# Kernel tuning notes

Measured on AMD Instinct MI355X. Metric: run time of the kernel, lower is better.

## Reference

```python
import jax, jax.numpy as jnp
import numpy as np

B, S, D = 2, 2048, 1024
H = 16
HD = D // H  # 64
SCALE = HD ** -0.5


def setup_inputs() -> dict:
    key = jax.random.key(0)
    ks = jax.random.split(key, 9)
    init = lambda k, shape: jax.random.normal(k, shape, dtype=jnp.float32) * (1.0 / np.sqrt(shape[-1]))
    return {
        "x": jax.random.normal(ks[0], (B, S, D), dtype=jnp.float32),
        "wq": init(ks[1], (D, D)), "bq": jnp.zeros((D,), jnp.float32),
        "wk": init(ks[2], (D, D)), "bk": jnp.zeros((D,), jnp.float32),
        "wv": init(ks[3], (D, D)), "bv": jnp.zeros((D,), jnp.float32),
        "wo": init(ks[4], (D, D)), "bo": jnp.zeros((D,), jnp.float32),
    }


def reference(x, wq, bq, wk, bk, wv, bv, wo, bo):
    b, s, d = x.shape
    # projections -> [b, h, s, hd]
    q = (x @ wq + bq).reshape(b, s, H, HD).transpose(0, 2, 1, 3)
    k = (x @ wk + bk).reshape(b, s, H, HD).transpose(0, 2, 1, 3)
    v = (x @ wv + bv).reshape(b, s, H, HD).transpose(0, 2, 1, 3)
    # full causal attention (chunked loop in original computes exactly this)
    scores = jnp.einsum("bhqd,bhkd->bhqk", q, k) * SCALE
    causal = jnp.tril(jnp.ones((s, s), dtype=bool))
    scores = jnp.where(causal, scores, -jnp.inf)
    weights = jax.nn.softmax(scores, axis=-1)
    out = jnp.einsum("bhqk,bhkd->bhqd", weights, v)
    out = out.transpose(0, 2, 1, 3).reshape(b, s, d)
    return out @ wo + bo
```

## Files before the change

### kernel.cpp

```cpp
#include <hip/hip_runtime.h>
#include <hip/hip_bf16.h>
#include <cstdint>

#define B_  2
#define S_  2048
#define D_  1024
#define H_  16
#define HD_ 64
#define M_  (B_ * S_)
static constexpr float SC_LOG2E = 0.125f * 1.44269504088896f;

typedef __bf16 bf16x8 __attribute__((ext_vector_type(8)));
typedef __bf16 bf16x4 __attribute__((ext_vector_type(4)));
typedef float  f32x4  __attribute__((ext_vector_type(4)));

__device__ __forceinline__ unsigned short f2b(float f) {
  union { float f; unsigned u; } x; x.f = f;
  unsigned r = x.u + 0x7FFF + ((x.u >> 16) & 1);
  return (unsigned short)(r >> 16);
}

__device__ __forceinline__ void gl_lds16(const unsigned short* g, unsigned short* l) {
  __builtin_amdgcn_global_load_lds((const __attribute__((address_space(1))) void*)g,
                                   (__attribute__((address_space(3))) void*)l, 16, 0, 0);
}

__device__ __forceinline__ void bar_lgkm() {
  asm volatile("s_waitcnt lgkmcnt(0)\n\ts_barrier" ::: "memory");
}
__device__ __forceinline__ void bar_vm2() {
  asm volatile("s_waitcnt vmcnt(2) lgkmcnt(0)\n\ts_barrier" ::: "memory");
}
__device__ __forceinline__ void bar_vm0() {
  asm volatile("s_waitcnt vmcnt(0) lgkmcnt(0)\n\ts_barrier" ::: "memory");
}

__global__ void cvt_all_kernel(const float* __restrict__ x,
                               const float* __restrict__ w0, const float* __restrict__ w1,
                               const float* __restrict__ w2, const float* __restrict__ w3,
                               unsigned short* __restrict__ xb,
                               unsigned short* __restrict__ o0, unsigned short* __restrict__ o1,
                               unsigned short* __restrict__ o2, unsigned short* __restrict__ o3) {
  int tx = threadIdx.x, ty = threadIdx.y;
  if (blockIdx.z == 4) {
    int tid = ty * 32 + tx;
    int base = ((int)blockIdx.y * 32 + (int)blockIdx.x) * 1024 + tid;
    const float4* xf = (const float4*)x;
    ushort4* ob = (ushort4*)xb;
#pragma unroll
    for (int j = 0; j < 4; j++) {
      float4 v = xf[base + j * 256];
      ushort4 r;
      r.x = f2b(v.x); r.y = f2b(v.y); r.z = f2b(v.z); r.w = f2b(v.w);
      ob[base + j * 256] = r;
    }
    return;
  }
  const float* w = blockIdx.z == 0 ? w0 : blockIdx.z == 1 ? w1 : blockIdx.z == 2 ? w2 : w3;
  unsigned short* o = blockIdx.z == 0 ? o0 : blockIdx.z == 1 ? o1 : blockIdx.z == 2 ? o2 : o3;
  __shared__ float t[32][33];
  int x0 = blockIdx.x * 32, y0 = blockIdx.y * 32;
#pragma unroll
  for (int j = 0; j < 4; j++)
    t[ty + j * 8][tx] = w[(size_t)(y0 + ty + j * 8) * D_ + x0 + tx];
  __syncthreads();
#pragma unroll
  for (int j = 0; j < 4; j++)
    o[(size_t)(x0 + ty + j * 8) * D_ + y0 + tx] = f2b(t[tx][ty + j * 8]);
}

__global__ __launch_bounds__(512) void qkv_gemm_kernel(
    const unsigned short* __restrict__ xb,
    const unsigned short* __restrict__ wqt, const unsigned short* __restrict__ wkt,
    const unsigned short* __restrict__ wvt,
    const float* __restrict__ bq, const float* __restrict__ bk, const float* __restrict__ bv,
    unsigned short* __restrict__ qo, unsigned short* __restrict__ ko, unsigned short* __restrict__ vo) {
  const unsigned short* wt = blockIdx.z == 0 ? wqt : blockIdx.z == 1 ? wkt : wvt;
  const float* bias        = blockIdx.z == 0 ? bq  : blockIdx.z == 1 ? bk  : bv;
  unsigned short* out      = blockIdx.z == 0 ? qo  : blockIdx.z == 1 ? ko  : vo;
  const float scl = blockIdx.z == 0 ? SC_LOG2E : 1.0f;

  __shared__ __align__(16) unsigned short smem[6 * 4096];
  const int tid = threadIdx.x;
  const int lane = tid & 63, wid = tid >> 6;
  const int wm = wid & 1, wn = wid >> 1;
  const int m0 = blockIdx.x * 128, n0 = blockIdx.y * 128;
  const int l15 = lane & 15, q4 = lane >> 4;
  const int srow = tid >> 2, skc = (tid & 3) * 8;

  f32x4 zero = {0.f, 0.f, 0.f, 0.f};
  f32x4 acc[4][2];
#pragma unroll
  for (int mt = 0; mt < 4; mt++)
#pragma unroll
    for (int nt = 0; nt < 2; nt++) acc[mt][nt] = zero;

  const unsigned short* ap = xb + (size_t)(m0 + srow) * D_ + skc;
  const unsigned short* bp = wt + (size_t)(n0 + srow) * D_ + skc;
  gl_lds16(ap,      smem + tid * 8);
  gl_lds16(bp,      smem + 12288 + tid * 8);
  gl_lds16(ap + 32, smem + 4096 + tid * 8);
  gl_lds16(bp + 32, smem + 12288 + 4096 + tid * 8);

  int bc = 0;
  for (int it = 0; it < 32; it++) {
    if (it < 31) bar_vm2(); else bar_vm0();
    if (it + 2 < 32) {
      int bn_ = bc < 1 ? bc + 2 : bc - 1;
      gl_lds16(ap + (it + 2) * 32, smem + bn_ * 4096 + tid * 8);
      gl_lds16(bp + (it + 2) * 32, smem + 12288 + bn_ * 4096 + tid * 8);
    }
    const unsigned short* Ab = smem + bc * 4096;
    const unsigned short* Bb = smem + 12288 + bc * 4096;
    bf16x8 af[4], bfv[2];
#pragma unroll
    for (int mt = 0; mt < 4; mt++) af[mt]  = *(const bf16x8*)(Ab + (wm * 64 + mt * 16 + l15) * 32 + q4 * 8);
#pragma unroll
    for (int nt = 0; nt < 2; nt++) bfv[nt] = *(const bf16x8*)(Bb + (wn * 32 + nt * 16 + l15) * 32 + q4 * 8);
#pragma unroll
    for (int mt = 0; mt < 4; mt++)
#pragma unroll
      for (int nt = 0; nt < 2; nt++)
        acc[mt][nt] = __builtin_amdgcn_mfma_f32_16x16x32_bf16(af[mt], bfv[nt], acc[mt][nt], 0, 0, 0);
    bc = bc == 2 ? 0 : bc + 1;
  }

  if (blockIdx.z < 2) {
#pragma unroll
    for (int nt = 0; nt < 2; nt++) {
      int n = n0 + wn * 32 + nt * 16 + l15;
      float bn = bias[n];
      int h = n >> 6, hd = n & 63;
#pragma unroll
      for (int mt = 0; mt < 4; mt++) {
#pragma unroll
        for (int r = 0; r < 4; r++) {
          int m = m0 + wm * 64 + mt * 16 + q4 * 4 + r;
          int b = m >> 11, s = m & (S_ - 1);
          out[(((size_t)(b * H_ + h)) * S_ + s) * HD_ + hd] = f2b((acc[mt][nt][r] + bn) * scl);
        }
      }
    }
  } else {
    unsigned short* buf = smem;
#pragma unroll
    for (int p = 0; p < 2; p++) {
      __syncthreads();
      if ((wn >> 1) == p) {
#pragma unroll
        for (int nt = 0; nt < 2; nt++) {
          int np = (wn & 1) * 32 + nt * 16 + l15;
          float bn = bias[n0 + p * 64 + np];
#pragma unroll
          for (int mt = 0; mt < 4; mt++) {
            f32x4 vb = acc[mt][nt];
            vb[0] += bn; vb[1] += bn; vb[2] += bn; vb[3] += bn;
            bf16x4 pk = __builtin_convertvector(vb, bf16x4);
            *(bf16x4*)(&buf[np * 136 + wm * 64 + mt * 16 + q4 * 4]) = pk;
          }
        }
      }
      __syncthreads();
#pragma unroll
      for (int i = 0; i < 2; i++) {
        int ci = tid + i * 512;
        int np = ci >> 4, c = ci & 15;
        int n = n0 + p * 64 + np;
        int h = n >> 6, hd = n & 63;
        int m = m0 + c * 8;
        int b = m >> 11, s = m & (S_ - 1);
        *(uint4*)(out + (((size_t)(b * H_ + h)) * HD_ + hd) * S_ + s) = *(const uint4*)(buf + np * 136 + c * 8);
      }
    }
  }
}

__global__ __launch_bounds__(512) void attn_kernel(
    const unsigned short* __restrict__ Q, const unsigned short* __restrict__ K,
    const unsigned short* __restrict__ Vt_g, unsigned short* __restrict__ O) {
  const int bh = blockIdx.y, b = bh >> 4, h = bh & 15;
  const unsigned short* Qh = Q    + (size_t)bh * S_ * HD_;
  const unsigned short* Kh = K    + (size_t)bh * S_ * HD_;
  const unsigned short* Vh = Vt_g + (size_t)bh * HD_ * S_;

  __shared__ __align__(16) unsigned short Ks[2][128 * 72];
  __shared__ __align__(16) unsigned short Vt[2][64 * 136];
  __shared__ __align__(16) unsigned short Ps[8][16 * 136];

  const int tid = threadIdx.x, lane = tid & 63, w = tid >> 6;
  const int l15 = lane & 15, q4 = lane >> 4;
  f32x4 zero = {0.f, 0.f, 0.f, 0.f};

  const int krow0 = tid >> 3, kcol0 = (tid & 7) * 8;
  const int vrow0 = tid >> 4, vcol0 = (tid & 15) * 8;

  int tc = 0;
  for (int half = 0; half < 2; half++) {
    const int qi = half ? (15 - (int)blockIdx.x) : (int)blockIdx.x;
    const int q0 = qi * 128;

    const unsigned short* qp = Qh + (size_t)(q0 + w * 16 + l15) * HD_ + q4 * 8;
    bf16x8 bq0 = *(const bf16x8*)(qp);
    bf16x8 bq1 = *(const bf16x8*)(qp + 32);

    float m_i = -1e30f, l_i = 0.f;
    f32x4 o_acc[4];
#pragma unroll
    for (int t = 0; t < 4; t++) o_acc[t] = zero;
    const int qrow = q0 + w * 16 + l15;
    const int nkt = qi + 1;

    uint4 kp0 = *(const uint4*)(Kh + (size_t)krow0 * HD_ + kcol0);
    uint4 kp1 = *(const uint4*)(Kh + (size_t)(krow0 + 64) * HD_ + kcol0);
    uint4 vp0 = *(const uint4*)(Vh + (size_t)vrow0 * S_ + vcol0);
    uint4 vp1 = *(const uint4*)(Vh + (size_t)(vrow0 + 32) * S_ + vcol0);

    for (int kt = 0; kt < nkt; kt++, tc++) {
      const int k0 = kt * 128;
      const int bi = tc & 1;
      unsigned short* Kb = Ks[bi];
      unsigned short* Vb = Vt[bi];
      *(uint4*)(Kb + krow0 * 72 + kcol0) = kp0;
      *(uint4*)(Kb + (krow0 + 64) * 72 + kcol0) = kp1;
      *(uint4*)(Vb + vrow0 * 136 + vcol0) = vp0;
      *(uint4*)(Vb + (vrow0 + 32) * 136 + vcol0) = vp1;
      bar_lgkm();
      if (kt + 1 < nkt) {
        int kn = k0 + 128;
        kp0 = *(const uint4*)(Kh + (size_t)(kn + krow0) * HD_ + kcol0);
        kp1 = *(const uint4*)(Kh + (size_t)(kn + krow0 + 64) * HD_ + kcol0);
        vp0 = *(const uint4*)(Vh + (size_t)vrow0 * S_ + kn + vcol0);
        vp1 = *(const uint4*)(Vh + (size_t)(vrow0 + 32) * S_ + kn + vcol0);
      }

      f32x4 sc[8];
#pragma unroll
      for (int nt = 0; nt < 8; nt++) sc[nt] = zero;
#pragma unroll
      for (int nt = 0; nt < 8; nt++) {
        bf16x8 ak0 = *(const bf16x8*)(Kb + (nt * 16 + l15) * 72 + q4 * 8);
        bf16x8 ak1 = *(const bf16x8*)(Kb + (nt * 16 + l15) * 72 + 32 + q4 * 8);
        sc[nt] = __builtin_amdgcn_mfma_f32_16x16x32_bf16(ak0, bq0, sc[nt], 0, 0, 0);
        sc[nt] = __builtin_amdgcn_mfma_f32_16x16x32_bf16(ak1, bq1, sc[nt], 0, 0, 0);
      }

      const bool needMask = (k0 + 127) > (q0 + w * 16);
      float mx = m_i;
      if (needMask) {
#pragma unroll
        for (int nt = 0; nt < 8; nt++)
#pragma unroll
          for (int r = 0; r < 4; r++) {
            int key = k0 + nt * 16 + q4 * 4 + r;
            float v = (key > qrow) ? -1e30f : sc[nt][r];
            sc[nt][r] = v;
            mx = fmaxf(mx, v);
          }
      } else {
#pragma unroll
        for (int nt = 0; nt < 8; nt++)
#pragma unroll
          for (int r = 0; r < 4; r++) mx = fmaxf(mx, sc[nt][r]);
      }
      mx = fmaxf(mx, __shfl_xor(mx, 16));
      mx = fmaxf(mx, __shfl_xor(mx, 32));
      float alpha = __builtin_amdgcn_exp2f(m_i - mx);
      m_i = mx;
      float rs = 0.f;
#pragma unroll
      for (int nt = 0; nt < 8; nt++)
#pragma unroll
        for (int r = 0; r < 4; r++) {
          float p = __builtin_amdgcn_exp2f(sc[nt][r] - mx);
          sc[nt][r] = p;
          rs += p;
        }
      rs += __shfl_xor(rs, 16);
      rs += __shfl_xor(rs, 32);
      l_i = l_i * alpha + rs;

#pragma unroll
      for (int r = 0; r < 4; r++) {
        float ar = __shfl(alpha, q4 * 4 + r);
        o_acc[0][r] *= ar; o_acc[1][r] *= ar; o_acc[2][r] *= ar; o_acc[3][r] *= ar;
      }

#pragma unroll
      for (int nt = 0; nt < 8; nt++) {
        bf16x4 pk = __builtin_convertvector(sc[nt], bf16x4);
        *(bf16x4*)(&Ps[w][l15 * 136 + nt * 16 + q4 * 4]) = pk;
      }
      __threadfence_block();

#pragma unroll
      for (int ks = 0; ks < 4; ks++) {
        bf16x8 ap = *(const bf16x8*)(&Ps[w][l15 * 136 + ks * 32 + q4 * 8]);
#pragma unroll
        for (int nt2 = 0; nt2 < 4; nt2++) {
          bf16x8 bv = *(const bf16x8*)(Vb + (nt2 * 16 + l15) * 136 + ks * 32 + q4 * 8);
          o_acc[nt2] = __builtin_amdgcn_mfma_f32_16x16x32_bf16(ap, bv, o_acc[nt2], 0, 0, 0);
        }
      }
    }

#pragma unroll
    for (int r = 0; r < 4; r++) {
      float lr = __shfl(l_i, q4 * 4 + r);
      float inv = 1.0f / lr;
      int s = q0 + w * 16 + q4 * 4 + r;
#pragma unroll
      for (int nt2 = 0; nt2 < 4; nt2++)
        O[((size_t)(b * S_ + s)) * D_ + h * HD_ + nt2 * 16 + l15] = f2b(o_acc[nt2][r] * inv);
    }
  }
}

__global__ __launch_bounds__(512) void out_gemm_kernel(
    const unsigned short* __restrict__ ab, const unsigned short* __restrict__ wot,
    const float* __restrict__ bo, float* __restrict__ out) {
  __shared__ __align__(16) unsigned short smem[6 * 4096];
  const int tid = threadIdx.x;
  const int lane = tid & 63, wid = tid >> 6;
  const int wm = wid & 1, wn = wid >> 1;
  const int m0 = blockIdx.x * 128, n0 = blockIdx.y * 128;
  const int l15 = lane & 15, q4 = lane >> 4;
  const int srow = tid >> 2, skc = (tid & 3) * 8;

  f32x4 zero = {0.f, 0.f, 0.f, 0.f};
  f32x4 acc[4][2];
#pragma unroll
  for (int mt = 0; mt < 4; mt++)
#pragma unroll
    for (int nt = 0; nt < 2; nt++) acc[mt][nt] = zero;

  const unsigned short* ap = ab  + (size_t)(m0 + srow) * D_ + skc;
  const unsigned short* bp = wot + (size_t)(n0 + srow) * D_ + skc;
  gl_lds16(ap,      smem + tid * 8);
  gl_lds16(bp,      smem + 12288 + tid * 8);
  gl_lds16(ap + 32, smem + 4096 + tid * 8);
  gl_lds16(bp + 32, smem + 12288 + 4096 + tid * 8);

  int bc = 0;
  for (int it = 0; it < 32; it++) {
    if (it < 31) bar_vm2(); else bar_vm0();
    if (it + 2 < 32) {
      int bn_ = bc < 1 ? bc + 2 : bc - 1;
      gl_lds16(ap + (it + 2) * 32, smem + bn_ * 4096 + tid * 8);
      gl_lds16(bp + (it + 2) * 32, smem + 12288 + bn_ * 4096 + tid * 8);
    }
    const unsigned short* Ab = smem + bc * 4096;
    const unsigned short* Bb = smem + 12288 + bc * 4096;
    bf16x8 af[4], bfv[2];
#pragma unroll
    for (int mt = 0; mt < 4; mt++) af[mt]  = *(const bf16x8*)(Ab + (wm * 64 + mt * 16 + l15) * 32 + q4 * 8);
#pragma unroll
    for (int nt = 0; nt < 2; nt++) bfv[nt] = *(const bf16x8*)(Bb + (wn * 32 + nt * 16 + l15) * 32 + q4 * 8);
#pragma unroll
    for (int mt = 0; mt < 4; mt++)
#pragma unroll
      for (int nt = 0; nt < 2; nt++)
        acc[mt][nt] = __builtin_amdgcn_mfma_f32_16x16x32_bf16(af[mt], bfv[nt], acc[mt][nt], 0, 0, 0);
    bc = bc == 2 ? 0 : bc + 1;
  }

#pragma unroll
  for (int nt = 0; nt < 2; nt++) {
    int n = n0 + wn * 32 + nt * 16 + l15;
    float bn = bo[n];
#pragma unroll
    for (int mt = 0; mt < 4; mt++) {
#pragma unroll
      for (int r = 0; r < 4; r++) {
        int m = m0 + wm * 64 + mt * 16 + q4 * 4 + r;
        out[(size_t)m * D_ + n] = acc[mt][nt][r] + bn;
      }
    }
  }
}

extern "C" void kernel_launch(void* const* d_in, const int* in_sizes, int n_in,
                              void* d_out, int out_size, void* d_ws, size_t ws_size,
                              hipStream_t stream) {
  const float* x  = (const float*)d_in[0];
  const float* wq = (const float*)d_in[1];
  const float* bq = (const float*)d_in[2];
  const float* wk = (const float*)d_in[3];
  const float* bk = (const float*)d_in[4];
  const float* wv = (const float*)d_in[5];
  const float* bv = (const float*)d_in[6];
  const float* wo = (const float*)d_in[7];
  const float* bo = (const float*)d_in[8];
  float* out = (float*)d_out;

  char* ws = (char*)d_ws;
  unsigned short* xb  = (unsigned short*)(ws);
  unsigned short* wqt = (unsigned short*)(ws + (8u  << 20));
  unsigned short* wkt = (unsigned short*)(ws + (10u << 20));
  unsigned short* wvt = (unsigned short*)(ws + (12u << 20));
  unsigned short* wot = (unsigned short*)(ws + (14u << 20));
  unsigned short* qb  = (unsigned short*)(ws + (16u << 20));
  unsigned short* kb  = (unsigned short*)(ws + (24u << 20));
  unsigned short* vtg = (unsigned short*)(ws + (32u << 20));
  unsigned short* ab  = xb;

  cvt_all_kernel<<<dim3(32, 32, 5), dim3(32, 8), 0, stream>>>(x, wq, wk, wv, wo, xb, wqt, wkt, wvt, wot);
  qkv_gemm_kernel<<<dim3(32, 8, 3), dim3(512), 0, stream>>>(xb, wqt, wkt, wvt, bq, bk, bv, qb, kb, vtg);
  attn_kernel<<<dim3(8, B_ * H_), dim3(512), 0, stream>>>(qb, kb, vtg, ab);
  out_gemm_kernel<<<dim3(32, 8), dim3(512), 0, stream>>>(ab, wot, bo, out);
}
```

Baseline: 180.3 us.

## Split attention KV tiles across two wave groups with merge, swizzled LDS

The attention kernel now launches 1024-thread blocks in which two groups of eight waves each process alternating 128-key tiles for the same query rows. Each group keeps its own online-softmax state, and the two states are merged through LDS scratch at the end. The change also XOR-swizzles the K/V LDS layout in place of padding, and skips the output rescale when the running max grows by less than a threshold. It interleaves the P stores with the PV MFMAs, adds s_setprio around MFMA blocks, and flattens the grid with head-major block ordering. The aim is to double key-dimension parallelism and cut LDS bank conflicts, at the cost of extra barriers, a merge step, and higher register and LDS pressure.

```diff
diff --git a/kernel.cpp b/kernel.cpp
--- a/kernel.cpp
+++ b/kernel.cpp
@@ -175,143 +175,206 @@
   }
 }
 
-__global__ __launch_bounds__(512) void attn_kernel(
+__global__ __launch_bounds__(1024, 4) void attn_kernel(
     const unsigned short* __restrict__ Q, const unsigned short* __restrict__ K,
     const unsigned short* __restrict__ Vt_g, unsigned short* __restrict__ O) {
-  const int bh = blockIdx.y, b = bh >> 4, h = bh & 15;
+  const int id = blockIdx.x;
+  const int bh = id & 31, x = id >> 5;
+  const int b = bh >> 4, h = bh & 15;
   const unsigned short* Qh = Q    + (size_t)bh * S_ * HD_;
   const unsigned short* Kh = K    + (size_t)bh * S_ * HD_;
   const unsigned short* Vh = Vt_g + (size_t)bh * HD_ * S_;
 
-  __shared__ __align__(16) unsigned short Ks[2][128 * 72];
-  __shared__ __align__(16) unsigned short Vt[2][64 * 136];
-  __shared__ __align__(16) unsigned short Ps[8][16 * 136];
+  __shared__ __align__(16) unsigned short Ks[2][2][128 * 64];
+  __shared__ __align__(16) unsigned short Vt[2][2][64 * 128];
+  __shared__ __align__(16) unsigned short Ps[16][640];
 
   const int tid = threadIdx.x, lane = tid & 63, w = tid >> 6;
+  const int hi = w >> 3, qw = w & 7;
   const int l15 = lane & 15, q4 = lane >> 4;
+  const int st = tid >> 9, sid = tid & 511;
+  const int krow0 = sid >> 3, kcol0 = (sid & 7) * 8;
+  const int vrow0 = sid >> 4, vcol0 = (sid & 15) * 8;
+  const int kc0s = kcol0 ^ ((krow0 & 7) << 3);
+  const int vc0s = vcol0 ^ ((vrow0 & 7) << 3);
+  const int kx = (l15 & 7) << 3;
+  const int kcA = (q4 * 8) ^ kx, kcB = (q4 * 8 + 32) ^ kx;
+  unsigned short* Pw = &Ps[w][0];
+  const int pw0 = l15 * 40 + q4 * 4;
+  const int pr0 = l15 * 40 + q4 * 8;
+  float* scr = (float*)&Ks[0][0][0];
+  float* sp = scr + (size_t)(qw * 64 + lane) * 20;
+
   f32x4 zero = {0.f, 0.f, 0.f, 0.f};
-
-  const int krow0 = tid >> 3, kcol0 = (tid & 7) * 8;
-  const int vrow0 = tid >> 4, vcol0 = (tid & 15) * 8;
-
-  int tc = 0;
-  for (int half = 0; half < 2; half++) {
-    const int qi = half ? (15 - (int)blockIdx.x) : (int)blockIdx.x;
+  int stc = 0;
+
+  for (int hf = 0; hf < 2; hf++) {
+    const int qi = hf ? 15 - x : x;
     const int q0 = qi * 128;
-
-    const unsigned short* qp = Qh + (size_t)(q0 + w * 16 + l15) * HD_ + q4 * 8;
+    const int nkt = qi + 1, nst = (nkt + 1) >> 1;
+
+    const unsigned short* qp = Qh + (size_t)(q0 + qw * 16 + l15) * HD_ + q4 * 8;
     bf16x8 bq0 = *(const bf16x8*)(qp);
     bf16x8 bq1 = *(const bf16x8*)(qp + 32);
+    const int qrow = q0 + qw * 16 + l15;
 
     float m_i = -1e30f, l_i = 0.f;
     f32x4 o_acc[4];
 #pragma unroll
-    for (int t = 0; t < 4; t++) o_acc[t] = zero;
-    const int qrow = q0 + w * 16 + l15;
-    const int nkt = qi + 1;
-
-    uint4 kp0 = *(const uint4*)(Kh + (size_t)krow0 * HD_ + kcol0);
-    uint4 kp1 = *(const uint4*)(Kh + (size_t)(krow0 + 64) * HD_ + kcol0);
-    uint4 vp0 = *(const uint4*)(Vh + (size_t)vrow0 * S_ + vcol0);
-    uint4 vp1 = *(const uint4*)(Vh + (size_t)(vrow0 + 32) * S_ + vcol0);
-
-    for (int kt = 0; kt < nkt; kt++, tc++) {
-      const int k0 = kt * 128;
-      const int bi = tc & 1;
-      unsigned short* Kb = Ks[bi];
-      unsigned short* Vb = Vt[bi];
-      *(uint4*)(Kb + krow0 * 72 + kcol0) = kp0;
-      *(uint4*)(Kb + (krow0 + 64) * 72 + kcol0) = kp1;
-      *(uint4*)(Vb + vrow0 * 136 + vcol0) = vp0;
-      *(uint4*)(Vb + (vrow0 + 32) * 136 + vcol0) = vp1;
+    for (int t4 = 0; t4 < 4; t4++) o_acc[t4] = zero;
+
+    uint4 kp0 = {0,0,0,0}, kp1 = {0,0,0,0}, vp0 = {0,0,0,0}, vp1 = {0,0,0,0};
+    if (st < nkt) {
+      const int k0p = st * 128;
+      kp0 = *(const uint4*)(Kh + (size_t)(k0p + krow0) * HD_ + kcol0);
+      kp1 = *(const uint4*)(Kh + (size_t)(k0p + krow0 + 64) * HD_ + kcol0);
+      vp0 = *(const uint4*)(Vh + (size_t)vrow0 * S_ + k0p + vcol0);
+      vp1 = *(const uint4*)(Vh + (size_t)(vrow0 + 32) * S_ + k0p + vcol0);
+    }
+
+    for (int s = 0; s < nst; s++, stc++) {
+      const int buf = stc & 1;
+      {
+        unsigned short* Kb = &Ks[buf][st][0];
+        unsigned short* Vb = &Vt[buf][st][0];
+        *(uint4*)(Kb + krow0 * 64 + kc0s) = kp0;
+        *(uint4*)(Kb + (krow0 + 64) * 64 + kc0s) = kp1;
+        *(uint4*)(Vb + vrow0 * 128 + vc0s) = vp0;
+        *(uint4*)(Vb + (vrow0 + 32) * 128 + vc0s) = vp1;
+      }
       bar_lgkm();
-      if (kt + 1 < nkt) {
-        int kn = k0 + 128;
-        kp0 = *(const uint4*)(Kh + (size_t)(kn + krow0) * HD_ + kcol0);
-        kp1 = *(const uint4*)(Kh + (size_t)(kn + krow0 + 64) * HD_ + kcol0);
-        vp0 = *(const uint4*)(Vh + (size_t)vrow0 * S_ + kn + vcol0);
-        vp1 = *(const uint4*)(Vh + (size_t)(vrow0 + 32) * S_ + kn + vcol0);
-      }
-
-      f32x4 sc[8];
-#pragma unroll
-      for (int nt = 0; nt < 8; nt++) sc[nt] = zero;
-#pragma unroll
-      for (int nt = 0; nt < 8; nt++) {
-        bf16x8 ak0 = *(const bf16x8*)(Kb + (nt * 16 + l15) * 72 + q4 * 8);
-        bf16x8 ak1 = *(const bf16x8*)(Kb + (nt * 16 + l15) * 72 + 32 + q4 * 8);
-        sc[nt] = __builtin_amdgcn_mfma_f32_16x16x32_bf16(ak0, bq0, sc[nt], 0, 0, 0);
-        sc[nt] = __builtin_amdgcn_mfma_f32_16x16x32_bf16(ak1, bq1, sc[nt], 0, 0, 0);
-      }
-
-      const bool needMask = (k0 + 127) > (q0 + w * 16);
-      float mx = m_i;
-      if (needMask) {
+      const int ktn = 2 * (s + 1) + st;
+      if (ktn < nkt) {
+        const int k0n = ktn * 128;
+        kp0 = *(const uint4*)(Kh + (size_t)(k0n + krow0) * HD_ + kcol0);
+        kp1 = *(const uint4*)(Kh + (size_t)(k0n + krow0 + 64) * HD_ + kcol0);
+        vp0 = *(const uint4*)(Vh + (size_t)vrow0 * S_ + k0n + vcol0);
+        vp1 = *(const uint4*)(Vh + (size_t)(vrow0 + 32) * S_ + k0n + vcol0);
+      }
+
+      const int kt = 2 * s + hi;
+      if (kt < nkt) {
+        const int k0 = kt * 128;
+        const unsigned short* Kb = &Ks[buf][hi][0];
+        const unsigned short* Vb = &Vt[buf][hi][0];
+
+        f32x4 sc[8];
+#pragma unroll
+        for (int nt = 0; nt < 8; nt++) sc[nt] = zero;
+        __builtin_amdgcn_s_setprio(1);
+#pragma unroll
+        for (int nt = 0; nt < 8; nt++) {
+          bf16x8 ak0 = *(const bf16x8*)(Kb + (nt * 16 + l15) * 64 + kcA);
+          bf16x8 ak1 = *(const bf16x8*)(Kb + (nt * 16 + l15) * 64 + kcB);
+          sc[nt] = __builtin_amdgcn_mfma_f32_16x16x32_bf16(ak0, bq0, sc[nt], 0, 0, 0);
+          sc[nt] = __builtin_amdgcn_mfma_f32_16x16x32_bf16(ak1, bq1, sc[nt], 0, 0, 0);
+        }
+        __builtin_amdgcn_s_setprio(0);
+
+        if ((k0 + 127) > (q0 + qw * 16)) {
+#pragma unroll
+          for (int nt = 0; nt < 8; nt++)
+#pragma unroll
+            for (int r = 0; r < 4; r++) {
+              int key = k0 + nt * 16 + q4 * 4 + r;
+              if (key > qrow) sc[nt][r] = -1e30f;
+            }
+        }
+
+        float am[8];
 #pragma unroll
         for (int nt = 0; nt < 8; nt++)
+          am[nt] = fmaxf(fmaxf(sc[nt][0], sc[nt][1]), fmaxf(sc[nt][2], sc[nt][3]));
+#pragma unroll
+        for (int sr = 4; sr > 0; sr >>= 1)
+#pragma unroll
+          for (int i2 = 0; i2 < sr; i2++) am[i2] = fmaxf(am[i2], am[i2 + sr]);
+        float mx = am[0];
+        mx = fmaxf(mx, __shfl_xor(mx, 16));
+        mx = fmaxf(mx, __shfl_xor(mx, 32));
+        mx = fmaxf(mx, m_i);
+
+        if (!__all(mx - m_i <= 10.0f)) {
+          float alpha = __builtin_amdgcn_exp2f(m_i - mx);
+          m_i = mx;
+          l_i *= alpha;
 #pragma unroll
           for (int r = 0; r < 4; r++) {
-            int key = k0 + nt * 16 + q4 * 4 + r;
-            float v = (key > qrow) ? -1e30f : sc[nt][r];
-            sc[nt][r] = v;
-            mx = fmaxf(mx, v);
+            float ar = __shfl(alpha, q4 * 4 + r);
+            o_acc[0][r] *= ar; o_acc[1][r] *= ar; o_acc[2][r] *= ar; o_acc[3][r] *= ar;
           }
-      } else {
-#pragma unroll
-        for (int nt = 0; nt < 8; nt++)
-#pragma unroll
-          for (int r = 0; r < 4; r++) mx = fmaxf(mx, sc[nt][r]);
-      }
-      mx = fmaxf(mx, __shfl_xor(mx, 16));
-      mx = fmaxf(mx, __shfl_xor(mx, 32));
-      float alpha = __builtin_amdgcn_exp2f(m_i - mx);
-      m_i = mx;
-      float rs = 0.f;
-#pragma unroll
-      for (int nt = 0; nt < 8; nt++)
-#pragma unroll
-        for (int r = 0; r < 4; r++) {
-          float p = __builtin_amdgcn_exp2f(sc[nt][r] - mx);
-          sc[nt][r] = p;
-          rs += p;
-        }
-      rs += __shfl_xor(rs, 16);
-      rs += __shfl_xor(rs, 32);
-      l_i = l_i * alpha + rs;
-
+        }
+
+        float sm[8];
+#pragma unroll
+        for (int nt = 0; nt < 8; nt++) {
+          f32x4 pv;
+#pragma unroll
+          for (int r = 0; r < 4; r++) pv[r] = __builtin_amdgcn_exp2f(sc[nt][r] - m_i);
+          sc[nt] = pv;
+          sm[nt] = (pv[0] + pv[1]) + (pv[2] + pv[3]);
+        }
+#pragma unroll
+        for (int sr = 4; sr > 0; sr >>= 1)
+#pragma unroll
+          for (int i2 = 0; i2 < sr; i2++) sm[i2] += sm[i2 + sr];
+        float rs = sm[0];
+        rs += __shfl_xor(rs, 16);
+        rs += __shfl_xor(rs, 32);
+        l_i += rs;
+
+#pragma unroll
+        for (int ks = 0; ks < 4; ks++) {
+          bf16x4 pk0 = __builtin_convertvector(sc[2 * ks],     bf16x4);
+          bf16x4 pk1 = __builtin_convertvector(sc[2 * ks + 1], bf16x4);
+          *(bf16x4*)(Pw + pw0)      = pk0;
+          *(bf16x4*)(Pw + pw0 + 16) = pk1;
+          __threadfence_block();
+          bf16x8 ap2 = *(const bf16x8*)(Pw + pr0);
+          __builtin_amdgcn_s_setprio(1);
+#pragma unroll
+          for (int nt2 = 0; nt2 < 4; nt2++) {
+            bf16x8 bv = *(const bf16x8*)(Vb + (nt2 * 16 + l15) * 128 + ((ks * 32 + q4 * 8) ^ kx));
+            o_acc[nt2] = __builtin_amdgcn_mfma_f32_16x16x32_bf16(ap2, bv, o_acc[nt2], 0, 0, 0);
+          }
+          __builtin_amdgcn_s_setprio(0);
+        }
+      }
+    }
+
+    bar_lgkm();
+    if (hi) {
+      *(f32x4*)(sp + 0)  = o_acc[0];
+      *(f32x4*)(sp + 4)  = o_acc[1];
+      *(f32x4*)(sp + 8)  = o_acc[2];
+      *(f32x4*)(sp + 12) = o_acc[3];
+      sp[16] = m_i; sp[17] = l_i;
+    }
+    bar_lgkm();
+    if (!hi) {
+      f32x4 oh[4];
+      oh[0] = *(const f32x4*)(sp + 0);
+      oh[1] = *(const f32x4*)(sp + 4);
+      oh[2] = *(const f32x4*)(sp + 8);
+      oh[3] = *(const f32x4*)(sp + 12);
+      float m_h = sp[16], l_h = sp[17];
+      float M   = fmaxf(m_i, m_h);
+      float a_l = __builtin_amdgcn_exp2f(m_i - M);
+      float a_h = __builtin_amdgcn_exp2f(m_h - M);
+      float l_f = l_i * a_l + l_h * a_h;
 #pragma unroll
       for (int r = 0; r < 4; r++) {
-        float ar = __shfl(alpha, q4 * 4 + r);
-        o_acc[0][r] *= ar; o_acc[1][r] *= ar; o_acc[2][r] *= ar; o_acc[3][r] *= ar;
-      }
-
-#pragma unroll
-      for (int nt = 0; nt < 8; nt++) {
-        bf16x4 pk = __builtin_convertvector(sc[nt], bf16x4);
-        *(bf16x4*)(&Ps[w][l15 * 136 + nt * 16 + q4 * 4]) = pk;
-      }
-      __threadfence_block();
-
-#pragma unroll
-      for (int ks = 0; ks < 4; ks++) {
-        bf16x8 ap = *(const bf16x8*)(&Ps[w][l15 * 136 + ks * 32 + q4 * 8]);
-#pragma unroll
-        for (int nt2 = 0; nt2 < 4; nt2++) {
-          bf16x8 bv = *(const bf16x8*)(Vb + (nt2 * 16 + l15) * 136 + ks * 32 + q4 * 8);
-          o_acc[nt2] = __builtin_amdgcn_mfma_f32_16x16x32_bf16(ap, bv, o_acc[nt2], 0, 0, 0);
-        }
-      }
-    }
-
-#pragma unroll
-    for (int r = 0; r < 4; r++) {
-      float lr = __shfl(l_i, q4 * 4 + r);
-      float inv = 1.0f / lr;
-      int s = q0 + w * 16 + q4 * 4 + r;
-#pragma unroll
-      for (int nt2 = 0; nt2 < 4; nt2++)
-        O[((size_t)(b * S_ + s)) * D_ + h * HD_ + nt2 * 16 + l15] = f2b(o_acc[nt2][r] * inv);
-    }
+        float arl = __shfl(a_l, q4 * 4 + r);
+        float arh = __shfl(a_h, q4 * 4 + r);
+        float inv = 1.0f / __shfl(l_f, q4 * 4 + r);
+        int s_ = q0 + qw * 16 + q4 * 4 + r;
+#pragma unroll
+        for (int nt2 = 0; nt2 < 4; nt2++)
+          O[((size_t)(b * S_ + s_)) * D_ + h * HD_ + nt2 * 16 + l15] =
+              f2b((o_acc[nt2][r] * arl + oh[nt2][r] * arh) * inv);
+      }
+    }
+    bar_lgkm();
   }
 }
 
@@ -405,6 +468,6 @@
 
   cvt_all_kernel<<<dim3(32, 32, 5), dim3(32, 8), 0, stream>>>(x, wq, wk, wv, wo, xb, wqt, wkt, wvt, wot);
   qkv_gemm_kernel<<<dim3(32, 8, 3), dim3(512), 0, stream>>>(xb, wqt, wkt, wvt, bq, bk, bv, qb, kb, vtg);
-  attn_kernel<<<dim3(8, B_ * H_), dim3(512), 0, stream>>>(qb, kb, vtg, ab);
+  attn_kernel<<<dim3(256), dim3(1024), 0, stream>>>(qb, kb, vtg, ab);
   out_gemm_kernel<<<dim3(32, 8), dim3(512), 0, stream>>>(ab, wot, bo, out);
 }
```

After: 180.1 us. No clear change (-0.1%).

## Restructure causal attention: one query tile per block, 64-key tiles, swizzled LDS

Applied to the files above, without the earlier changes.

The attention kernel now launches 512 blocks, each handling a single 128-row query tile, replacing 256 blocks that each processed a balanced pair of tiles. Blocks are ordered so that long and short causal tiles interleave. Key tiles shrink to 64 rows and are stored in XOR-swizzled unpadded LDS, which cuts shared memory use so that four blocks can be resident per CU. The kernel also skips fully masked tiles per wave, rescales the running max only when it grows by more than a threshold (a lazy rescale), and raises wave priority around the MFMA sections. The trade-off is more blocks and barriers, shorter inner loops, and possible load imbalance across blocks.

```diff
diff --git a/kernel.cpp b/kernel.cpp
--- a/kernel.cpp
+++ b/kernel.cpp
@@ -175,143 +175,156 @@
   }
 }
 
-__global__ __launch_bounds__(512) void attn_kernel(
+__global__ __launch_bounds__(512, 4) void attn_kernel(
     const unsigned short* __restrict__ Q, const unsigned short* __restrict__ K,
     const unsigned short* __restrict__ Vt_g, unsigned short* __restrict__ O) {
-  const int bh = blockIdx.y, b = bh >> 4, h = bh & 15;
+  const int id = blockIdx.x;
+  const int u = id >> 8, v = id & 255;
+  const int bh = v & 31;
+  const int t = v >> 5;
+  const int qi = u ? (15 - t) : t;
+  const int b = bh >> 4, h = bh & 15;
   const unsigned short* Qh = Q    + (size_t)bh * S_ * HD_;
   const unsigned short* Kh = K    + (size_t)bh * S_ * HD_;
   const unsigned short* Vh = Vt_g + (size_t)bh * HD_ * S_;
 
-  __shared__ __align__(16) unsigned short Ks[2][128 * 72];
-  __shared__ __align__(16) unsigned short Vt[2][64 * 136];
-  __shared__ __align__(16) unsigned short Ps[8][16 * 136];
+  __shared__ __align__(16) unsigned short Ks[2][64 * 64];
+  __shared__ __align__(16) unsigned short Vt[2][64 * 64];
+  __shared__ __align__(16) unsigned short Ps[8][16 * 72];
 
   const int tid = threadIdx.x, lane = tid & 63, w = tid >> 6;
   const int l15 = lane & 15, q4 = lane >> 4;
+  const int kx = (l15 & 7) << 3;
+  const int kcA = (q4 * 8) ^ kx, kcB = (q4 * 8 + 32) ^ kx;
+  const int vc0 = (q4 * 8) ^ kx, vc1 = (32 + q4 * 8) ^ kx;
+  unsigned short* Pw = &Ps[w][0];
+
+  const int srow = tid >> 3;
+  const int scolS = (((tid & 7) ^ (srow & 7)) * 8);
+  const unsigned short* kg = Kh + (size_t)srow * HD_ + (tid & 7) * 8;
+  const unsigned short* vg = Vh + (size_t)srow * S_  + (tid & 7) * 8;
+
+  const int q0 = qi * 128;
+  const int nkt = 2 * qi + 2;
+  const int qlo = q0 + w * 16;
+  const int qmax = qlo + 15;
+  const int qrow = qlo + l15;
+
+  const unsigned short* qp = Qh + (size_t)qrow * HD_ + q4 * 8;
+  bf16x8 bq0 = *(const bf16x8*)(qp);
+  bf16x8 bq1 = *(const bf16x8*)(qp + 32);
+
+  float m_i = -1e30f, l_i = 0.f;
   f32x4 zero = {0.f, 0.f, 0.f, 0.f};
-
-  const int krow0 = tid >> 3, kcol0 = (tid & 7) * 8;
-  const int vrow0 = tid >> 4, vcol0 = (tid & 15) * 8;
-
-  int tc = 0;
-  for (int half = 0; half < 2; half++) {
-    const int qi = half ? (15 - (int)blockIdx.x) : (int)blockIdx.x;
-    const int q0 = qi * 128;
-
-    const unsigned short* qp = Qh + (size_t)(q0 + w * 16 + l15) * HD_ + q4 * 8;
-    bf16x8 bq0 = *(const bf16x8*)(qp);
-    bf16x8 bq1 = *(const bf16x8*)(qp + 32);
-
-    float m_i = -1e30f, l_i = 0.f;
-    f32x4 o_acc[4];
-#pragma unroll
-    for (int t = 0; t < 4; t++) o_acc[t] = zero;
-    const int qrow = q0 + w * 16 + l15;
-    const int nkt = qi + 1;
-
-    uint4 kp0 = *(const uint4*)(Kh + (size_t)krow0 * HD_ + kcol0);
-    uint4 kp1 = *(const uint4*)(Kh + (size_t)(krow0 + 64) * HD_ + kcol0);
-    uint4 vp0 = *(const uint4*)(Vh + (size_t)vrow0 * S_ + vcol0);
-    uint4 vp1 = *(const uint4*)(Vh + (size_t)(vrow0 + 32) * S_ + vcol0);
-
-    for (int kt = 0; kt < nkt; kt++, tc++) {
-      const int k0 = kt * 128;
-      const int bi = tc & 1;
-      unsigned short* Kb = Ks[bi];
-      unsigned short* Vb = Vt[bi];
-      *(uint4*)(Kb + krow0 * 72 + kcol0) = kp0;
-      *(uint4*)(Kb + (krow0 + 64) * 72 + kcol0) = kp1;
-      *(uint4*)(Vb + vrow0 * 136 + vcol0) = vp0;
-      *(uint4*)(Vb + (vrow0 + 32) * 136 + vcol0) = vp1;
-      bar_lgkm();
-      if (kt + 1 < nkt) {
-        int kn = k0 + 128;
-        kp0 = *(const uint4*)(Kh + (size_t)(kn + krow0) * HD_ + kcol0);
-        kp1 = *(const uint4*)(Kh + (size_t)(kn + krow0 + 64) * HD_ + kcol0);
-        vp0 = *(const uint4*)(Vh + (size_t)vrow0 * S_ + kn + vcol0);
-        vp1 = *(const uint4*)(Vh + (size_t)(vrow0 + 32) * S_ + kn + vcol0);
-      }
-
-      f32x4 sc[8];
-#pragma unroll
-      for (int nt = 0; nt < 8; nt++) sc[nt] = zero;
-#pragma unroll
-      for (int nt = 0; nt < 8; nt++) {
-        bf16x8 ak0 = *(const bf16x8*)(Kb + (nt * 16 + l15) * 72 + q4 * 8);
-        bf16x8 ak1 = *(const bf16x8*)(Kb + (nt * 16 + l15) * 72 + 32 + q4 * 8);
+  f32x4 o_acc[4];
+#pragma unroll
+  for (int t4 = 0; t4 < 4; t4++) o_acc[t4] = zero;
+
+  uint4 kp = *(const uint4*)(kg);
+  uint4 vp = *(const uint4*)(vg);
+
+  for (int kt = 0; kt < nkt; kt++) {
+    const int k0 = kt * 64;
+    unsigned short* Kb = Ks[kt & 1];
+    unsigned short* Vb = Vt[kt & 1];
+    *(uint4*)(Kb + srow * 64 + scolS) = kp;
+    *(uint4*)(Vb + srow * 64 + scolS) = vp;
+    bar_lgkm();
+    if (kt + 1 < nkt) {
+      kp = *(const uint4*)(kg + (size_t)(kt + 1) * 64 * HD_);
+      vp = *(const uint4*)(vg + (kt + 1) * 64);
+    }
+
+    if (k0 <= qmax) {
+      f32x4 sc[4];
+#pragma unroll
+      for (int nt = 0; nt < 4; nt++) sc[nt] = zero;
+      __builtin_amdgcn_s_setprio(1);
+#pragma unroll
+      for (int nt = 0; nt < 4; nt++) {
+        bf16x8 ak0 = *(const bf16x8*)(Kb + (nt * 16 + l15) * 64 + kcA);
+        bf16x8 ak1 = *(const bf16x8*)(Kb + (nt * 16 + l15) * 64 + kcB);
         sc[nt] = __builtin_amdgcn_mfma_f32_16x16x32_bf16(ak0, bq0, sc[nt], 0, 0, 0);
         sc[nt] = __builtin_amdgcn_mfma_f32_16x16x32_bf16(ak1, bq1, sc[nt], 0, 0, 0);
       }
-
-      const bool needMask = (k0 + 127) > (q0 + w * 16);
-      float mx = m_i;
-      if (needMask) {
-#pragma unroll
-        for (int nt = 0; nt < 8; nt++)
+      __builtin_amdgcn_s_setprio(0);
+
+      if ((k0 + 63) > qlo) {
+#pragma unroll
+        for (int nt = 0; nt < 4; nt++)
 #pragma unroll
           for (int r = 0; r < 4; r++) {
             int key = k0 + nt * 16 + q4 * 4 + r;
-            float v = (key > qrow) ? -1e30f : sc[nt][r];
-            sc[nt][r] = v;
-            mx = fmaxf(mx, v);
+            if (key > qrow) sc[nt][r] = -1e30f;
           }
-      } else {
-#pragma unroll
-        for (int nt = 0; nt < 8; nt++)
-#pragma unroll
-          for (int r = 0; r < 4; r++) mx = fmaxf(mx, sc[nt][r]);
-      }
+      }
+
+      float am[4];
+#pragma unroll
+      for (int nt = 0; nt < 4; nt++)
+        am[nt] = fmaxf(fmaxf(sc[nt][0], sc[nt][1]), fmaxf(sc[nt][2], sc[nt][3]));
+      am[0] = fmaxf(am[0], am[2]); am[1] = fmaxf(am[1], am[3]);
+      float mx = fmaxf(am[0], am[1]);
       mx = fmaxf(mx, __shfl_xor(mx, 16));
       mx = fmaxf(mx, __shfl_xor(mx, 32));
-      float alpha = __builtin_amdgcn_exp2f(m_i - mx);
-      m_i = mx;
-      float rs = 0.f;
-#pragma unroll
-      for (int nt = 0; nt < 8; nt++)
+      mx = fmaxf(mx, m_i);
+
+      if (!__all(mx - m_i <= 10.0f)) {
+        float alpha = __builtin_amdgcn_exp2f(m_i - mx);
+        m_i = mx;
+        l_i *= alpha;
 #pragma unroll
         for (int r = 0; r < 4; r++) {
-          float p = __builtin_amdgcn_exp2f(sc[nt][r] - mx);
-          sc[nt][r] = p;
-          rs += p;
+          float ar = __shfl(alpha, q4 * 4 + r);
+          o_acc[0][r] *= ar; o_acc[1][r] *= ar; o_acc[2][r] *= ar; o_acc[3][r] *= ar;
         }
+      }
+
+      float sm[4];
+#pragma unroll
+      for (int nt = 0; nt < 4; nt++) {
+        f32x4 pv;
+#pragma unroll
+        for (int r = 0; r < 4; r++) pv[r] = __builtin_amdgcn_exp2f(sc[nt][r] - m_i);
+        sc[nt] = pv;
+        sm[nt] = (pv[0] + pv[1]) + (pv[2] + pv[3]);
+      }
+      float rs = (sm[0] + sm[2]) + (sm[1] + sm[3]);
       rs += __shfl_xor(rs, 16);
       rs += __shfl_xor(rs, 32);
-      l_i = l_i * alpha + rs;
-
-#pragma unroll
-      for (int r = 0; r < 4; r++) {
-        float ar = __shfl(alpha, q4 * 4 + r);
-        o_acc[0][r] *= ar; o_acc[1][r] *= ar; o_acc[2][r] *= ar; o_acc[3][r] *= ar;
-      }
-
-#pragma unroll
-      for (int nt = 0; nt < 8; nt++) {
+      l_i += rs;
+
+#pragma unroll
+      for (int nt = 0; nt < 4; nt++) {
         bf16x4 pk = __builtin_convertvector(sc[nt], bf16x4);
-        *(bf16x4*)(&Ps[w][l15 * 136 + nt * 16 + q4 * 4]) = pk;
+        *(bf16x4*)(Pw + l15 * 72 + nt * 16 + q4 * 4) = pk;
       }
       __threadfence_block();
-
-#pragma unroll
-      for (int ks = 0; ks < 4; ks++) {
-        bf16x8 ap = *(const bf16x8*)(&Ps[w][l15 * 136 + ks * 32 + q4 * 8]);
-#pragma unroll
-        for (int nt2 = 0; nt2 < 4; nt2++) {
-          bf16x8 bv = *(const bf16x8*)(Vb + (nt2 * 16 + l15) * 136 + ks * 32 + q4 * 8);
-          o_acc[nt2] = __builtin_amdgcn_mfma_f32_16x16x32_bf16(ap, bv, o_acc[nt2], 0, 0, 0);
-        }
-      }
-    }
-
-#pragma unroll
-    for (int r = 0; r < 4; r++) {
-      float lr = __shfl(l_i, q4 * 4 + r);
-      float inv = 1.0f / lr;
-      int s = q0 + w * 16 + q4 * 4 + r;
-#pragma unroll
-      for (int nt2 = 0; nt2 < 4; nt2++)
-        O[((size_t)(b * S_ + s)) * D_ + h * HD_ + nt2 * 16 + l15] = f2b(o_acc[nt2][r] * inv);
-    }
+      bf16x8 ap0 = *(const bf16x8*)(Pw + l15 * 72 + q4 * 8);
+      bf16x8 ap1 = *(const bf16x8*)(Pw + l15 * 72 + 32 + q4 * 8);
+      __builtin_amdgcn_s_setprio(1);
+#pragma unroll
+      for (int nt2 = 0; nt2 < 4; nt2++) {
+        bf16x8 bv0 = *(const bf16x8*)(Vb + (nt2 * 16 + l15) * 64 + vc0);
+        o_acc[nt2] = __builtin_amdgcn_mfma_f32_16x16x32_bf16(ap0, bv0, o_acc[nt2], 0, 0, 0);
+      }
+#pragma unroll
+      for (int nt2 = 0; nt2 < 4; nt2++) {
+        bf16x8 bv1 = *(const bf16x8*)(Vb + (nt2 * 16 + l15) * 64 + vc1);
+        o_acc[nt2] = __builtin_amdgcn_mfma_f32_16x16x32_bf16(ap1, bv1, o_acc[nt2], 0, 0, 0);
+      }
+      __builtin_amdgcn_s_setprio(0);
+    }
+  }
+
+#pragma unroll
+  for (int r = 0; r < 4; r++) {
+    float lr = __shfl(l_i, q4 * 4 + r);
+    float inv = 1.0f / lr;
+    int s_ = q0 + w * 16 + q4 * 4 + r;
+#pragma unroll
+    for (int nt2 = 0; nt2 < 4; nt2++)
+      O[((size_t)(b * S_ + s_)) * D_ + h * HD_ + nt2 * 16 + l15] = f2b(o_acc[nt2][r] * inv);
   }
 }
 
@@ -405,6 +418,6 @@
 
   cvt_all_kernel<<<dim3(32, 32, 5), dim3(32, 8), 0, stream>>>(x, wq, wk, wv, wo, xb, wqt, wkt, wvt, wot);
   qkv_gemm_kernel<<<dim3(32, 8, 3), dim3(512), 0, stream>>>(xb, wqt, wkt, wvt, bq, bk, bv, qb, kb, vtg);
-  attn_kernel<<<dim3(8, B_ * H_), dim3(512), 0, stream>>>(qb, kb, vtg, ab);
+  attn_kernel<<<dim3(512), dim3(512), 0, stream>>>(qb, kb, vtg, ab);
   out_gemm_kernel<<<dim3(32, 8), dim3(512), 0, stream>>>(ab, wot, bo, out);
 }
```

After: 181.7 us. Within noise of the previous version (+0.8%).
